# Kernel tuning notes

Measured on AMD Instinct MI355X. Metric: run time of the kernel, lower is better.

Reference implementation:

```python
import jax, jax.numpy as jnp
import numpy as np

D_MODEL = 1024
NUM_HEADS = 16
D_K = D_MODEL // NUM_HEADS
MAX_SEQ_LEN = 2048
THETA = 10000.0


def setup_inputs() -> dict:
    key = jax.random.key(0)
    k0, k1, k2, k3, k4 = jax.random.split(key, 5)
    B, S = 2, 2048
    std = (2.0 / (D_MODEL + D_MODEL)) ** 0.5
    # trunc_normal with std=std*std approximated by normal scaled (same distributional scale)
    w = lambda k: (std * std) * jax.random.truncated_normal(k, -3.0 / std, 3.0 / std, (D_MODEL, D_MODEL), jnp.float32)
    return {
        "in_features": jax.random.normal(k0, (B, S, D_MODEL), jnp.float32),
        "token_positions": jnp.arange(S, dtype=jnp.int32),
        "Wq": w(k1), "Wk": w(k2), "Wv": w(k3), "Wo": w(k4),
    }


def _rope(x, token_positions):
    # x: [B, H, S, d_k]; interleaved even/odd rotation
    freq = 1.0 / jnp.power(THETA, jnp.arange(0, D_K, 2, dtype=jnp.float32) / D_K)
    pos = jnp.arange(MAX_SEQ_LEN, dtype=jnp.float32)
    freqs = jnp.outer(pos, freq)                      # [max_seq, d_k/2]
    cos = jnp.cos(freqs)[token_positions]             # [S, d_k/2]
    sin = jnp.sin(freqs)[token_positions]
    even, odd = x[..., 0::2], x[..., 1::2]
    even_out = even * cos - odd * sin
    odd_out = even * sin + odd * cos
    return jnp.stack([even_out, odd_out], axis=-1).reshape(x.shape)


def reference(in_features, token_positions, Wq, Wk, Wv, Wo):
    B, S, _ = in_features.shape
    split = lambda t: t.reshape(B, S, NUM_HEADS, D_K).transpose(0, 2, 1, 3)  # [B,H,S,d_k]
    q = split(in_features @ Wq.T)
    k = split(in_features @ Wk.T)
    v = split(in_features @ Wv.T)
    q = _rope(q, token_positions)
    k = _rope(k, token_positions)
    score = jnp.einsum('bhqd,bhkd->bhqk', q, k) / jnp.sqrt(jnp.float32(D_K))
    mask = jnp.tril(jnp.ones((S, S), dtype=bool))
    score = jnp.where(mask, score, -jnp.inf)
    attn = jax.nn.softmax(score, axis=-1)
    out = jnp.einsum('bhqk,bhkd->bhqd', attn, v)       # [B,H,S,d_k]
    out = out.transpose(0, 2, 1, 3).reshape(B, S, D_MODEL)
    return out @ Wo.T
```

## Files before the change

### kernel.cpp

```cpp
#include <hip/hip_runtime.h>
#include <stdint.h>


typedef unsigned short u16;
typedef __bf16 bf16x8 __attribute__((ext_vector_type(8)));
typedef float f32x4 __attribute__((ext_vector_type(4)));
typedef u16 u16x4 __attribute__((ext_vector_type(4)));

#define LOG2E 1.44269504088896340736f
#define QSCALE (0.125f * LOG2E)

static __device__ __forceinline__ u16 f2bf(float f) {
  __bf16 b = (__bf16)f;
  return __builtin_bit_cast(u16, b);
}

template<bool F32>
static __device__ __forceinline__ bf16x8 load8(const void* p, size_t off) {
  if constexpr (F32) {
    const float* f = (const float*)p + off;
    f32x4 a = *(const f32x4*)f;
    f32x4 b = *(const f32x4*)(f + 4);
    bf16x8 r;
    r[0] = (__bf16)a[0]; r[1] = (__bf16)a[1]; r[2] = (__bf16)a[2]; r[3] = (__bf16)a[3];
    r[4] = (__bf16)b[0]; r[5] = (__bf16)b[1]; r[6] = (__bf16)b[2]; r[7] = (__bf16)b[3];
    return r;
  } else {
    return *(const bf16x8*)((const u16*)p + off);
  }
}

static __device__ __forceinline__ void glds16(const u16* g, u16* l) {
  __builtin_amdgcn_global_load_lds(
      (const __attribute__((address_space(1))) unsigned int*)g,
      (__attribute__((address_space(3))) unsigned int*)l, 16, 0, 0);
}

__global__ void cvt_bf16_kernel(const float* __restrict__ in,
                                u16* __restrict__ out, int n8) {
  int i = blockIdx.x * 256 + threadIdx.x;
  if (i >= n8) return;
  const float* p = in + (size_t)i * 8;
  f32x4 a = *(const f32x4*)p;
  f32x4 b = *(const f32x4*)(p + 4);
  bf16x8 r;
  r[0] = (__bf16)a[0]; r[1] = (__bf16)a[1]; r[2] = (__bf16)a[2]; r[3] = (__bf16)a[3];
  r[4] = (__bf16)b[0]; r[5] = (__bf16)b[1]; r[6] = (__bf16)b[2]; r[7] = (__bf16)b[3];
  *(bf16x8*)(out + (size_t)i * 8) = r;
}

__global__ void prep_kernel(const float* __restrict__ Wq, const float* __restrict__ Wk,
                            const float* __restrict__ Wv, const float* __restrict__ Wo,
                            u16* __restrict__ out,
                            const int* __restrict__ tp,
                            float* __restrict__ cosT, float* __restrict__ sinT) {
  const int z = blockIdx.z;
  if (z == 4) {
    int idx = blockIdx.x * 256 + threadIdx.x;
    if (idx >= 2048 * 32) return;
    int s = idx >> 5, i = idx & 31;
    float p = (float)tp[s];
    float freq = powf(10000.0f, -(float)i / 32.0f);
    float ang = p * freq;
    cosT[idx] = cosf(ang);
    sinT[idx] = sinf(ang);
    return;
  }
  const float* src = (z == 0) ? Wq : (z == 1) ? Wk : (z == 2) ? Wv : Wo;
  u16* dst = out + (size_t)z * 1024 * 1024;
  int i = blockIdx.x * 256 + threadIdx.x;
  if (i >= 1024 * 1024 / 8) return;
  const float* p = src + (size_t)i * 8;
  f32x4 a = *(const f32x4*)p;
  f32x4 b = *(const f32x4*)(p + 4);
  bf16x8 r;
  r[0] = (__bf16)a[0]; r[1] = (__bf16)a[1]; r[2] = (__bf16)a[2]; r[3] = (__bf16)a[3];
  r[4] = (__bf16)b[0]; r[5] = (__bf16)b[1]; r[6] = (__bf16)b[2]; r[7] = (__bf16)b[3];
  *(bf16x8*)(dst + (size_t)i * 8) = r;
}

template<bool AF32, bool BF32>
static __device__ __forceinline__ void gemm128_core(
    const void* __restrict__ A, const void* __restrict__ W,
    u16* As, u16* Bs, int m0, int n0, f32x4 (&acc)[4][4]) {
  const int tid = threadIdx.x;
  const int lane = tid & 63;
  const int wave = tid >> 6;
  const int wr = (wave >> 1) * 64, wc = (wave & 1) * 64;
  const int lr = lane & 15, lg = lane >> 4;
  const int srow = tid >> 3;
  const int scol = ((tid & 7) ^ (srow & 7)) * 8;
  for (int k0 = 0; k0 < 1024; k0 += 64) {
    if constexpr (!AF32 && !BF32) {
      const u16* Ab = (const u16*)A;
      const u16* Wb = (const u16*)W;
      __syncthreads();
#pragma unroll
      for (int i = 0; i < 4; ++i) {
        glds16(Ab + (size_t)(m0 + srow + i * 32) * 1024 + k0 + scol, As + tid * 8 + i * 2048);
        glds16(Wb + (size_t)(n0 + srow + i * 32) * 1024 + k0 + scol, Bs + tid * 8 + i * 2048);
      }
      __syncthreads();
    } else {
      bf16x8 ta[4], tb[4];
#pragma unroll
      for (int i = 0; i < 4; ++i) {
        ta[i] = load8<AF32>(A, (size_t)(m0 + srow + i * 32) * 1024 + k0 + scol);
        tb[i] = load8<BF32>(W, (size_t)(n0 + srow + i * 32) * 1024 + k0 + scol);
      }
      __syncthreads();
#pragma unroll
      for (int i = 0; i < 4; ++i) {
        *(bf16x8*)(As + tid * 8 + i * 2048) = ta[i];
        *(bf16x8*)(Bs + tid * 8 + i * 2048) = tb[i];
      }
      __syncthreads();
    }
#pragma unroll
    for (int kk = 0; kk < 2; ++kk) {
      bf16x8 af[4], bfr[4];
#pragma unroll
      for (int i = 0; i < 4; ++i) {
        const int ga = ((kk * 4 + lg) ^ (lr & 7)) * 8;
        af[i]  = *(const bf16x8*)(As + (wr + i * 16 + lr) * 64 + ga);
        bfr[i] = *(const bf16x8*)(Bs + (wc + i * 16 + lr) * 64 + ga);
      }
#pragma unroll
      for (int i = 0; i < 4; ++i)
#pragma unroll
        for (int j = 0; j < 4; ++j)
          acc[i][j] = __builtin_amdgcn_mfma_f32_16x16x32_bf16(af[i], bfr[j], acc[i][j], 0, 0, 0);
    }
  }
}

template<bool F32>
__global__ __launch_bounds__(256, 3)
void qkv_gemm_kernel(const void* __restrict__ X,
                     const void* __restrict__ Wq, const void* __restrict__ Wk,
                     const void* __restrict__ Wv,
                     const float* __restrict__ cosT, const float* __restrict__ sinT,
                     u16* __restrict__ Qo, u16* __restrict__ Ko, u16* __restrict__ Vto) {
  __shared__ __align__(16) u16 As[128 * 64];
  __shared__ __align__(16) u16 Bs[128 * 64];
  const int z = blockIdx.z;
  const void* W = (z == 0) ? Wq : ((z == 1) ? Wk : Wv);
  const int m0 = blockIdx.x * 128, n0 = blockIdx.y * 128;
  f32x4 acc[4][4] = {};
  gemm128_core<F32, F32>(X, W, As, Bs, m0, n0, acc);
  const int lane = threadIdx.x & 63, wave = threadIdx.x >> 6;
  const int wr = (wave >> 1) * 64, wc = (wave & 1) * 64;
  const int lr = lane & 15, lg = lane >> 4;
  if (z < 2) {
    u16* dst = z ? Ko : Qo;
    const float qs = z ? 1.0f : QSCALE;
    const int parity = lr & 1;
#pragma unroll
    for (int i = 0; i < 4; ++i) {
      const int rb = m0 + wr + i * 16 + lg * 4;
#pragma unroll
      for (int n = 0; n < 4; ++n) {
        const int c = n0 + wc + n * 16 + lr;
        const int hh = c >> 6, d = c & 63;
        const int ifr = d >> 1;
#pragma unroll
        for (int j = 0; j < 4; ++j) {
          const int r = rb + j;
          const int s = r & 2047;
          float v = acc[i][n][j];
          float p = __shfl_xor(v, 1);
          float cs = cosT[s * 32 + ifr];
          float sn = sinT[s * 32 + ifr];
          float res = parity ? (p * sn + v * cs) : (v * cs - p * sn);
          dst[(((size_t)(r >> 11) * 16 + hh) * 2048 + s) * 64 + d] =
              f2bf(res * qs);
        }
      }
    }
  } else {
#pragma unroll
    for (int i = 0; i < 4; ++i) {
      const int s0 = m0 + wr + i * 16 + lg * 4;
      const int bb = s0 >> 11, ss = s0 & 2047;
#pragma unroll
      for (int n = 0; n < 4; ++n) {
        const int c = n0 + wc + n * 16 + lr;
        const int hh = c >> 6, d = c & 63;
        u16x4 pk;
#pragma unroll
        for (int j = 0; j < 4; ++j) pk[j] = f2bf(acc[i][n][j]);
        *(u16x4*)(Vto + (((size_t)bb * 16 + hh) * 64 + d) * 2048 + ss) = pk;
      }
    }
  }
}

template<bool MASKED>
static __device__ __forceinline__ void attn_tile(
    const u16* kb, const u16* vb, int kv0, int qrow,
    const bf16x8 (&qf)[2], u16* Psw,
    f32x4 (&accO)[4], float& m, float& l, int lr, int lg) {
  f32x4 sacc[4] = {};
  __builtin_amdgcn_s_setprio(1);
#pragma unroll
  for (int n = 0; n < 4; ++n)
#pragma unroll
    for (int kk = 0; kk < 2; ++kk) {
      const int gsw = ((((kk << 2) | lg) ^ (lr & 7)) << 3);
      bf16x8 kf = *(const bf16x8*)&kb[(n * 16 + lr) * 64 + gsw];
      sacc[n] = __builtin_amdgcn_mfma_f32_16x16x32_bf16(kf, qf[kk], sacc[n], 0, 0, 0);
    }
  __builtin_amdgcn_s_setprio(0);
  if (MASKED) {
#pragma unroll
    for (int n = 0; n < 4; ++n)
#pragma unroll
      for (int j = 0; j < 4; ++j) {
        const int c = kv0 + n * 16 + lg * 4 + j;
        if (c > qrow) sacc[n][j] = -1e30f;
      }
  }
  float t0 = fmaxf(fmaxf(sacc[0][0], sacc[0][1]), sacc[0][2]);
  float t1 = fmaxf(fmaxf(sacc[0][3], sacc[1][0]), sacc[1][1]);
  float t2 = fmaxf(fmaxf(sacc[1][2], sacc[1][3]), sacc[2][0]);
  float t3 = fmaxf(fmaxf(sacc[2][1], sacc[2][2]), sacc[2][3]);
  float t4 = fmaxf(fmaxf(sacc[3][0], sacc[3][1]), sacc[3][2]);
  float tm = fmaxf(fmaxf(t0, t1), fmaxf(fmaxf(t2, t3), fmaxf(t4, sacc[3][3])));
  tm = fmaxf(tm, __shfl_xor(tm, 16));
  tm = fmaxf(tm, __shfl_xor(tm, 32));

  float ssum = 0.f;
  u16x4 pk[4];
  if (__all(tm <= m + 8.0f)) {
#pragma unroll
    for (int n = 0; n < 4; ++n)
#pragma unroll
      for (int j = 0; j < 4; ++j) {
        float p = exp2f(sacc[n][j] - m);
        ssum += p;
        pk[n][j] = f2bf(p);
      }
    ssum += __shfl_xor(ssum, 16);
    ssum += __shfl_xor(ssum, 32);
    l += ssum;
  } else {
    const float mn = fmaxf(m, tm);
    const float al = exp2f(m - mn);
    m = mn;
#pragma unroll
    for (int n = 0; n < 4; ++n)
#pragma unroll
      for (int j = 0; j < 4; ++j) {
        float p = exp2f(sacc[n][j] - mn);
        ssum += p;
        pk[n][j] = f2bf(p);
      }
    ssum += __shfl_xor(ssum, 16);
    ssum += __shfl_xor(ssum, 32);
    l = l * al + ssum;
#pragma unroll
    for (int n = 0; n < 4; ++n)
#pragma unroll
      for (int j = 0; j < 4; ++j)
        accO[n][j] *= al;
  }
#pragma unroll
  for (int n = 0; n < 4; ++n) {
    const int g = n * 4 + lg;
    const int off = ((((g >> 1) ^ (lr & 7)) << 3) | ((g & 1) << 2));
    *(u16x4*)&Psw[lr * 64 + off] = pk[n];
  }
  __builtin_amdgcn_s_setprio(1);
#pragma unroll
  for (int kk = 0; kk < 2; ++kk) {
    const int po = (((kk * 4 + lg) ^ (lr & 7)) << 3);
    bf16x8 pb = *(const bf16x8*)&Psw[lr * 64 + po];
#pragma unroll
    for (int db = 0; db < 4; ++db) {
      const int gsw = ((((kk << 2) | lg) ^ (lr & 7)) << 3);
      bf16x8 vf = *(const bf16x8*)&vb[(db * 16 + lr) * 64 + gsw];
      accO[db] = __builtin_amdgcn_mfma_f32_16x16x32_bf16(vf, pb, accO[db], 0, 0, 0);
    }
  }
  __builtin_amdgcn_s_setprio(0);
}

__global__ __launch_bounds__(256, 4)
void flash_attn_kernel(const u16* __restrict__ Q, const u16* __restrict__ K,
                       const u16* __restrict__ Vt, u16* __restrict__ O) {
  __shared__ __align__(16) u16 Klds[2][64 * 64];
  __shared__ __align__(16) u16 Vlds[2][64 * 64];
  __shared__ __align__(16) u16 Ps[4][16 * 64];
  const int bh = blockIdx.x;
  const int qcb = 31 - (int)blockIdx.y;
  const int b = bh >> 4, h = bh & 15;
  const int tid = threadIdx.x;
  const int wv = tid >> 6, lane = tid & 63;
  const int lr = lane & 15, lg = lane >> 4;
  const int qbase = qcb * 64 + wv * 16;
  const int qrow = qbase + lr;
  const size_t hb = (size_t)bh * (2048 * 64);
  const u16* Qh = Q + hb;
  const u16* Kh = K + hb;
  const u16* Vh = Vt + hb;

  const int sgr = ((lane & 7) ^ (lane >> 3)) << 3;
  const int srw = lane >> 3;
  auto STAGE = [&](int kv0, int bufi) {
    u16* kbd = Klds[bufi];
    u16* vbd = Vlds[bufi];
#pragma unroll
    for (int i = 0; i < 2; ++i) {
      const int r = wv * 16 + i * 8;
      glds16(Kh + (size_t)(kv0 + r + srw) * 64 + sgr, kbd + r * 64);
      glds16(Vh + (size_t)(r + srw) * 2048 + kv0 + sgr, vbd + r * 64);
    }
  };

  bf16x8 qf[2];
#pragma unroll
  for (int kk = 0; kk < 2; ++kk)
    qf[kk] = *(const bf16x8*)(Qh + (size_t)qrow * 64 + kk * 32 + lg * 8);

  f32x4 accO[4] = {};
  float m = -1e30f, l = 0.f;

  const int nt = qcb + 1;
  STAGE(0, 0);
  __syncthreads();
  for (int t = 0; t < nt - 1; ++t) {
    STAGE((t + 1) * 64, (t & 1) ^ 1);
    attn_tile<false>(Klds[t & 1], Vlds[t & 1], t * 64, qrow, qf, Ps[wv],
                     accO, m, l, lr, lg);
    __syncthreads();
  }
  attn_tile<true>(Klds[(nt - 1) & 1], Vlds[(nt - 1) & 1], (nt - 1) * 64, qrow,
                  qf, Ps[wv], accO, m, l, lr, lg);

  const float inv = 1.0f / l;
#pragma unroll
  for (int db = 0; db < 4; ++db) {
    u16x4 pk;
#pragma unroll
    for (int j = 0; j < 4; ++j) pk[j] = f2bf(accO[db][j] * inv);
    const int d = db * 16 + lg * 4;
    *(u16x4*)&O[((size_t)(b * 2048 + qrow) * 16 + h) * 64 + d] = pk;
  }
}

template<bool WF32>
__global__ __launch_bounds__(256, 2)
void out_gemm_kernel(const u16* __restrict__ A, const void* __restrict__ W,
                     float* __restrict__ out) {
  __shared__ __align__(16) u16 As[128 * 64];
  __shared__ __align__(16) u16 Bs[128 * 64];
  const int m0 = blockIdx.x * 128, n0 = blockIdx.y * 128;
  f32x4 acc[4][4] = {};
  gemm128_core<false, WF32>(A, W, As, Bs, m0, n0, acc);
  const int lane = threadIdx.x & 63, wave = threadIdx.x >> 6;
  const int wr = (wave >> 1) * 64, wc = (wave & 1) * 64;
  const int lr = lane & 15, lg = lane >> 4;
#pragma unroll
  for (int i = 0; i < 4; ++i)
#pragma unroll
    for (int n = 0; n < 4; ++n) {
      const int c = n0 + wc + n * 16 + lr;
#pragma unroll
      for (int j = 0; j < 4; ++j) {
        const int r = m0 + wr + i * 16 + lg * 4 + j;
        out[(size_t)r * 1024 + c] = acc[i][n][j];
      }
    }
}

extern "C" void kernel_launch(void* const* d_in, const int* in_sizes, int n_in,
                              void* d_out, int out_size, void* d_ws, size_t ws_size,
                              hipStream_t stream) {
  const float* x  = (const float*)d_in[0];
  const int*   tp = (const int*)d_in[1];
  const float* Wq = (const float*)d_in[2];
  const float* Wk = (const float*)d_in[3];
  const float* Wv = (const float*)d_in[4];
  const float* Wo = (const float*)d_in[5];
  float* out = (float*)d_out;
  const int B = in_sizes[0] / (2048 * 1024);
  const size_t xel = (size_t)B * 2048 * 1024;
  const size_t tsz = xel * sizeof(u16);
  const size_t TBL = 2048 * 32 * 2 * sizeof(float);
  u16* Qb = (u16*)d_out;
  u16* Kb = (u16*)((char*)d_out + tsz);
  char* ws = (char*)d_ws;
  u16* Vt = (u16*)(ws);
  u16* Ob = (u16*)(ws + tsz);
  float* cosT = (float*)(ws + 2 * tsz);
  float* sinT = cosT + 2048 * 32;
  u16* Xb  = (u16*)(ws + 2 * tsz + TBL);
  u16* Wb4 = Xb + xel;
  const size_t need = 2 * tsz + TBL + tsz + 4 * (size_t)(1024 * 1024) * sizeof(u16);
  const bool cvt = ws_size >= need;

  if (cvt) {
    prep_kernel<<<dim3(512, 1, 5), dim3(256), 0, stream>>>(
        Wq, Wk, Wv, Wo, Wb4, tp, cosT, sinT);
    cvt_bf16_kernel<<<dim3((int)(xel / 8 / 256)), dim3(256), 0, stream>>>(x, Xb, (int)(xel / 8));
    qkv_gemm_kernel<false><<<dim3(B * 16, 8, 3), dim3(256), 0, stream>>>(
        Xb, Wb4, Wb4 + 1024 * 1024, Wb4 + 2 * 1024 * 1024, cosT, sinT, Qb, Kb, Vt);
  } else {
    prep_kernel<<<dim3(512, 1, 5), dim3(256), 0, stream>>>(
        Wq, Wk, Wv, Wo, Wb4, tp, cosT, sinT);
    qkv_gemm_kernel<true><<<dim3(B * 16, 8, 3), dim3(256), 0, stream>>>(
        x, Wq, Wk, Wv, cosT, sinT, Qb, Kb, Vt);
  }
  flash_attn_kernel<<<dim3(B * 16, 32), dim3(256), 0, stream>>>(Qb, Kb, Vt, Ob);
  if (cvt) {
    out_gemm_kernel<false><<<dim3(B * 16, 8), dim3(256), 0, stream>>>(
        Ob, Wb4 + 3 * 1024 * 1024, out);
  } else {
    out_gemm_kernel<true><<<dim3(B * 16, 8), dim3(256), 0, stream>>>(Ob, Wo, out);
  }
}
```

Before: 111.4 us.

## Fuse input conversion into prep kernel, use native exp2, simplify KV staging addressing

Merges the separate fp32-to-bf16 conversion of the input activations into the weight/rope prep kernel as extra z-planes, removing one kernel launch. Replaces exp2f in the attention softmax with the hardware native exp2 instruction, avoiding the range-reduction wrapper. Rewrites the K/V staging address computation to use incrementing pointers instead of recomputing offsets each tile. The native exp2 may lose a little accuracy or handle denormals differently.

```diff
diff --git a/kernel.cpp b/kernel.cpp
--- a/kernel.cpp
+++ b/kernel.cpp
@@ -13,6 +13,15 @@
 static __device__ __forceinline__ u16 f2bf(float f) {
   __bf16 b = (__bf16)f;
   return __builtin_bit_cast(u16, b);
+}
+
+extern "C" __device__ float __ocml_native_exp2_f32(float);
+static __device__ __forceinline__ float fexp2(float x) {
+#if __has_builtin(__builtin_amdgcn_exp2f)
+  return __builtin_amdgcn_exp2f(x);
+#else
+  return __ocml_native_exp2_f32(x);
+#endif
 }
 
 template<bool F32>
@@ -36,47 +45,47 @@
       (__attribute__((address_space(3))) unsigned int*)l, 16, 0, 0);
 }
 
-__global__ void cvt_bf16_kernel(const float* __restrict__ in,
-                                u16* __restrict__ out, int n8) {
-  int i = blockIdx.x * 256 + threadIdx.x;
-  if (i >= n8) return;
-  const float* p = in + (size_t)i * 8;
+__global__ void prep_kernel(const float* __restrict__ Wq, const float* __restrict__ Wk,
+                            const float* __restrict__ Wv, const float* __restrict__ Wo,
+                            u16* __restrict__ wout,
+                            const float* __restrict__ x, u16* __restrict__ xout,
+                            size_t xn8,
+                            const int* __restrict__ tp,
+                            float* __restrict__ cosT, float* __restrict__ sinT) {
+  const int z = blockIdx.z;
+  const int i = blockIdx.x * 256 + threadIdx.x;
+  if (z == 4) {
+    if (i >= 2048 * 32) return;
+    int s = i >> 5, fi = i & 31;
+    float p = (float)tp[s];
+    float freq = powf(10000.0f, -(float)fi / 32.0f);
+    float ang = p * freq;
+    cosT[i] = cosf(ang);
+    sinT[i] = sinf(ang);
+    return;
+  }
+  const float* src;
+  u16* dst;
+  size_t off;
+  if (z < 4) {
+    if (i >= 1024 * 1024 / 8) return;
+    src = (z == 0) ? Wq : (z == 1) ? Wk : (z == 2) ? Wv : Wo;
+    dst = wout + (size_t)z * 1024 * 1024;
+    off = (size_t)i * 8;
+  } else {
+    size_t gi = (size_t)(z - 5) * (512 * 256) + i;
+    if (gi >= xn8) return;
+    src = x;
+    dst = xout;
+    off = gi * 8;
+  }
+  const float* p = src + off;
   f32x4 a = *(const f32x4*)p;
   f32x4 b = *(const f32x4*)(p + 4);
   bf16x8 r;
   r[0] = (__bf16)a[0]; r[1] = (__bf16)a[1]; r[2] = (__bf16)a[2]; r[3] = (__bf16)a[3];
   r[4] = (__bf16)b[0]; r[5] = (__bf16)b[1]; r[6] = (__bf16)b[2]; r[7] = (__bf16)b[3];
-  *(bf16x8*)(out + (size_t)i * 8) = r;
-}
-
-__global__ void prep_kernel(const float* __restrict__ Wq, const float* __restrict__ Wk,
-                            const float* __restrict__ Wv, const float* __restrict__ Wo,
-                            u16* __restrict__ out,
-                            const int* __restrict__ tp,
-                            float* __restrict__ cosT, float* __restrict__ sinT) {
-  const int z = blockIdx.z;
-  if (z == 4) {
-    int idx = blockIdx.x * 256 + threadIdx.x;
-    if (idx >= 2048 * 32) return;
-    int s = idx >> 5, i = idx & 31;
-    float p = (float)tp[s];
-    float freq = powf(10000.0f, -(float)i / 32.0f);
-    float ang = p * freq;
-    cosT[idx] = cosf(ang);
-    sinT[idx] = sinf(ang);
-    return;
-  }
-  const float* src = (z == 0) ? Wq : (z == 1) ? Wk : (z == 2) ? Wv : Wo;
-  u16* dst = out + (size_t)z * 1024 * 1024;
-  int i = blockIdx.x * 256 + threadIdx.x;
-  if (i >= 1024 * 1024 / 8) return;
-  const float* p = src + (size_t)i * 8;
-  f32x4 a = *(const f32x4*)p;
-  f32x4 b = *(const f32x4*)(p + 4);
-  bf16x8 r;
-  r[0] = (__bf16)a[0]; r[1] = (__bf16)a[1]; r[2] = (__bf16)a[2]; r[3] = (__bf16)a[3];
-  r[4] = (__bf16)b[0]; r[5] = (__bf16)b[1]; r[6] = (__bf16)b[2]; r[7] = (__bf16)b[3];
-  *(bf16x8*)(dst + (size_t)i * 8) = r;
+  *(bf16x8*)(dst + off) = r;
 }
 
 template<bool AF32, bool BF32>
@@ -236,7 +245,7 @@
     for (int n = 0; n < 4; ++n)
 #pragma unroll
       for (int j = 0; j < 4; ++j) {
-        float p = exp2f(sacc[n][j] - m);
+        float p = fexp2(sacc[n][j] - m);
         ssum += p;
         pk[n][j] = f2bf(p);
       }
@@ -245,13 +254,13 @@
     l += ssum;
   } else {
     const float mn = fmaxf(m, tm);
-    const float al = exp2f(m - mn);
+    const float al = fexp2(m - mn);
     m = mn;
 #pragma unroll
     for (int n = 0; n < 4; ++n)
 #pragma unroll
       for (int j = 0; j < 4; ++j) {
-        float p = exp2f(sacc[n][j] - mn);
+        float p = fexp2(sacc[n][j] - mn);
         ssum += p;
         pk[n][j] = f2bf(p);
       }
@@ -301,20 +310,19 @@
   const int qrow = qbase + lr;
   const size_t hb = (size_t)bh * (2048 * 64);
   const u16* Qh = Q + hb;
-  const u16* Kh = K + hb;
-  const u16* Vh = Vt + hb;
 
   const int sgr = ((lane & 7) ^ (lane >> 3)) << 3;
   const int srw = lane >> 3;
-  auto STAGE = [&](int kv0, int bufi) {
-    u16* kbd = Klds[bufi];
-    u16* vbd = Vlds[bufi];
-#pragma unroll
-    for (int i = 0; i < 2; ++i) {
-      const int r = wv * 16 + i * 8;
-      glds16(Kh + (size_t)(kv0 + r + srw) * 64 + sgr, kbd + r * 64);
-      glds16(Vh + (size_t)(r + srw) * 2048 + kv0 + sgr, vbd + r * 64);
-    }
+  const u16* kp = K + hb + (size_t)(wv * 16 + srw) * 64 + sgr;
+  const u16* vp = Vt + hb + (size_t)(wv * 16 + srw) * 2048 + sgr;
+  const int ldso = (wv * 16) * 64;
+  auto STAGE = [&](const u16* kq, const u16* vq, int bufi) {
+    u16* kbd = Klds[bufi] + ldso;
+    u16* vbd = Vlds[bufi] + ldso;
+    glds16(kq, kbd);
+    glds16(kq + 8 * 64, kbd + 8 * 64);
+    glds16(vq, vbd);
+    glds16(vq + 8 * 2048, vbd + 8 * 64);
   };
 
   bf16x8 qf[2];
@@ -326,10 +334,12 @@
   float m = -1e30f, l = 0.f;
 
   const int nt = qcb + 1;
-  STAGE(0, 0);
+  STAGE(kp, vp, 0);
+  kp += 64 * 64; vp += 64;
   __syncthreads();
   for (int t = 0; t < nt - 1; ++t) {
-    STAGE((t + 1) * 64, (t & 1) ^ 1);
+    STAGE(kp, vp, (t & 1) ^ 1);
+    kp += 64 * 64; vp += 64;
     attn_tile<false>(Klds[t & 1], Vlds[t & 1], t * 64, qrow, qf, Ps[wv],
                      accO, m, l, lr, lg);
     __syncthreads();
@@ -398,16 +408,17 @@
   u16* Wb4 = Xb + xel;
   const size_t need = 2 * tsz + TBL + tsz + 4 * (size_t)(1024 * 1024) * sizeof(u16);
   const bool cvt = ws_size >= need;
+  const size_t xn8 = xel / 8;
+  const int xplanes = (int)((xn8 + 512 * 256 - 1) / (512 * 256));
 
   if (cvt) {
-    prep_kernel<<<dim3(512, 1, 5), dim3(256), 0, stream>>>(
-        Wq, Wk, Wv, Wo, Wb4, tp, cosT, sinT);
-    cvt_bf16_kernel<<<dim3((int)(xel / 8 / 256)), dim3(256), 0, stream>>>(x, Xb, (int)(xel / 8));
+    prep_kernel<<<dim3(512, 1, 5 + xplanes), dim3(256), 0, stream>>>(
+        Wq, Wk, Wv, Wo, Wb4, x, Xb, xn8, tp, cosT, sinT);
     qkv_gemm_kernel<false><<<dim3(B * 16, 8, 3), dim3(256), 0, stream>>>(
         Xb, Wb4, Wb4 + 1024 * 1024, Wb4 + 2 * 1024 * 1024, cosT, sinT, Qb, Kb, Vt);
   } else {
     prep_kernel<<<dim3(512, 1, 5), dim3(256), 0, stream>>>(
-        Wq, Wk, Wv, Wo, Wb4, tp, cosT, sinT);
+        Wq, Wk, Wv, Wo, Wb4, x, Xb, 0, tp, cosT, sinT);
     qkv_gemm_kernel<true><<<dim3(B * 16, 8, 3), dim3(256), 0, stream>>>(
         x, Wq, Wk, Wv, cosT, sinT, Qb, Kb, Vt);
   }
```

After: 103.2 us. 1.08x faster.
